# Kernel tuning notes

Measured on AMD Instinct MI355X. Metric: run time of the kernel, lower is better.

The kernel has to match this reference:

```python
import jax, jax.numpy as jnp
import numpy as np

E = 128       # embed_size
H = 256       # hidden_size
Q = 256       # query_size
B = 256       # batch size
N_ENT = 200000
N_REL = 500
N_NODES = 100000   # existing (head) nodes
N_NEW = 50000      # new tail nodes (segment_sum size)
M = 200000         # edges


def setup_inputs() -> dict:
    key = jax.random.key(0)
    ks = jax.random.split(key, 32)
    s = 0.02
    inp = {
        'entity_emb':   jax.random.normal(ks[0], (N_ENT, E), jnp.float32),
        'relation_emb': jax.random.normal(ks[1], (N_REL, E), jnp.float32),
        'node_hidden':  jax.random.normal(ks[2], (N_NODES, H), jnp.float32),
        'query_repr':   jax.random.normal(ks[3], (B, Q), jnp.float32),
        # attention params (Ws_attn, Wr_attn, Wqr_attn, w_alpha)
        'Ws':  jax.random.normal(ks[4], (H, H), jnp.float32) * s,
        'Wr':  jax.random.normal(ks[5], (E, H), jnp.float32) * s,
        'Wqr': jax.random.normal(ks[6], (E, H), jnp.float32) * s,
        'bqr': jnp.zeros((H,), jnp.float32),
        'w_alpha': jax.random.normal(ks[7], (H, 1), jnp.float32) * s,
        'b_alpha': jnp.zeros((1,), jnp.float32),
        # GRUCell (input = 2E message, hidden = H), torch layout [3H, in]
        'W_ih': jax.random.normal(ks[8], (3 * H, 2 * E), jnp.float32) * s,
        'W_hh': jax.random.normal(ks[9], (3 * H, H), jnp.float32) * s,
        'b_ih': jnp.zeros((3 * H,), jnp.float32),
        'b_hh': jnp.zeros((3 * H,), jnp.float32),
        # We2h: entity embed -> initial hidden
        'We2h_W': jax.random.normal(ks[10], (E, H), jnp.float32) * s,
        'We2h_b': jnp.zeros((H,), jnp.float32),
        # candidate_layer: [2E + H] -> H (agent_num = 1)
        'cand_W': jax.random.normal(ks[11], (2 * E + H, H), jnp.float32) * s,
        'cand_b': jnp.zeros((H,), jnp.float32),
        # rank_layer: [H + Q] -> 1
        'rank_W': jax.random.normal(ks[12], (H + Q, 1), jnp.float32) * s,
        'rank_b': jnp.zeros((1,), jnp.float32),
        # LayerNorm
        'ln_g': jnp.ones((H,), jnp.float32),
        'ln_b': jnp.zeros((H,), jnp.float32),
        # edge list (int constants)
        'head_node':     jax.random.randint(ks[13], (M,), 0, N_NODES, jnp.int32),
        'edge_rel':      jax.random.randint(ks[14], (M,), 0, N_REL, jnp.int32),
        'tail_ent':      jax.random.randint(ks[15], (M,), 0, N_ENT, jnp.int32),
        'tail_node':     jax.random.randint(ks[16], (M,), 0, N_NEW, jnp.int32),
        'query_rel':     jax.random.randint(ks[17], (M,), 0, N_REL, jnp.int32),
        'batch_idx':     jax.random.randint(ks[18], (M,), 0, B, jnp.int32),
        'tail_node_ent': jax.random.randint(ks[19], (N_NEW,), 0, N_ENT, jnp.int32),
    }
    return inp


def reference(entity_emb, relation_emb, node_hidden, query_repr,
              Ws, Wr, Wqr, bqr, w_alpha, b_alpha,
              W_ih, W_hh, b_ih, b_hh, We2h_W, We2h_b,
              cand_W, cand_b, rank_W, rank_b, ln_g, ln_b,
              head_node, edge_rel, tail_ent, tail_node, query_rel,
              batch_idx, tail_node_ent):
    lrelu = lambda x: jax.nn.leaky_relu(x, 0.01)
    # --- per-edge attention: w_alpha(ReLU(Ws h_s + Wr h_r + Wqr h_q)) ---
    hs = node_hidden[head_node]            # [M, H]
    hr = relation_emb[edge_rel]            # [M, E]
    hq = relation_emb[query_rel]           # [M, E]
    attn_feat = jax.nn.relu(hs @ Ws + hr @ Wr + hq @ Wqr + bqr)   # [M, H]
    alpha = jax.nn.sigmoid(attn_feat @ w_alpha + b_alpha)         # [M, 1]
    # --- attention-weighted message (rel || tail entity) scattered to tails ---
    te = entity_emb[tail_ent]                                     # [M, E]
    msg = jnp.concatenate([hr, te], axis=-1) * alpha              # [M, 2E]
    agg = jax.ops.segment_sum(msg, tail_node, num_segments=N_NEW) # [N_NEW, 2E]
    # --- GRUCell update of tail-node hidden states ---
    h_prev = lrelu(entity_emb[tail_node_ent] @ We2h_W + We2h_b)   # [N_NEW, H]
    gx = agg @ W_ih.T + b_ih                                      # [N_NEW, 3H]
    gh = h_prev @ W_hh.T + b_hh
    xr, xz, xn = jnp.split(gx, 3, axis=-1)
    hr_, hz_, hn_ = jnp.split(gh, 3, axis=-1)
    r = jax.nn.sigmoid(xr + hr_)
    z = jax.nn.sigmoid(xz + hz_)
    n = jnp.tanh(xn + r * hn_)
    h_new = (1.0 - z) * n + z * h_prev                            # [N_NEW, H]
    mu = jnp.mean(h_new, axis=-1, keepdims=True)
    var = jnp.var(h_new, axis=-1, keepdims=True)
    h_new = (h_new - mu) * jax.lax.rsqrt(var + 1e-5) * ln_g + ln_b
    # --- candidate scoring: candidate_layer + rank_layer ---
    cand_in = jnp.concatenate([te, hr, h_new[tail_node]], axis=-1)   # [M, 2E+H]
    cand_h = lrelu(cand_in @ cand_W + cand_b)                        # [M, H]
    rank_in = jnp.concatenate([cand_h, query_repr[batch_idx]], -1)   # [M, H+Q]
    scores = (rank_in @ rank_W + rank_b)[:, 0]                       # [M]
    return scores
```

## Files before the change

### kernel.cpp

```cpp
#include <hip/hip_runtime.h>
#include <math.h>


#define ACT_NONE 0
#define ACT_LRELU 1

typedef __attribute__((ext_vector_type(8))) short short8;
typedef __attribute__((ext_vector_type(4))) float floatx4;

__device__ __forceinline__ ushort f2b(float x) {
    union { float f; unsigned u; } v; v.f = x;
    return (ushort)((v.u + 0x7fffu + ((v.u >> 16) & 1u)) >> 16);
}
__device__ __forceinline__ float b2f(ushort b) {
    union { unsigned u; float f; } v; v.u = ((unsigned)b) << 16;
    return v.f;
}
__device__ __forceinline__ void gload16(const ushort* g, ushort* l) {
    __builtin_amdgcn_global_load_lds(
        (const __attribute__((address_space(1))) void*)g,
        (__attribute__((address_space(3))) void*)l, 16, 0, 0);
}

__global__ __launch_bounds__(256) void relprep_k(
    const float* __restrict__ A, const float* __restrict__ B0,
    const float* __restrict__ B1, const float* __restrict__ B2,
    float* __restrict__ C0, float* __restrict__ C1, ushort* __restrict__ C2,
    int M, int N, int K)
{
    __shared__ float As[16][68];
    __shared__ float Bs[16][68];
    const int z = blockIdx.z;
    const float* B = (z == 0) ? B0 : (z == 1) ? B1 : B2;
    const int tid = threadIdx.x;
    const int tx = tid & 15, ty = tid >> 4;
    const int m0 = blockIdx.x * 64, n0 = blockIdx.y * 64;
    float acc[4][4] = {};
    const int ar  = tid >> 2;
    const int ac4 = (tid & 3) * 4;
    const int brow = tid >> 4;
    const int bc4  = (tid & 15) * 4;
    const int gm = m0 + ar;
    const float* Arow = (gm < M) ? (A + (size_t)gm * K) : nullptr;
    for (int k0 = 0; k0 < K; k0 += 16) {
        float4 av = make_float4(0.f, 0.f, 0.f, 0.f);
        if (Arow) av = *(const float4*)(Arow + k0 + ac4);
        As[ac4 + 0][ar] = av.x;
        As[ac4 + 1][ar] = av.y;
        As[ac4 + 2][ar] = av.z;
        As[ac4 + 3][ar] = av.w;
        float4 bv = *(const float4*)(B + (size_t)(k0 + brow) * N + n0 + bc4);
        *(float4*)&Bs[brow][bc4] = bv;
        __syncthreads();
        #pragma unroll
        for (int kk = 0; kk < 16; ++kk) {
            float4 a4 = *(float4*)&As[kk][ty << 2];
            float4 b4 = *(float4*)&Bs[kk][tx << 2];
            float avr[4] = {a4.x, a4.y, a4.z, a4.w};
            float bvr[4] = {b4.x, b4.y, b4.z, b4.w};
            #pragma unroll
            for (int i = 0; i < 4; ++i)
                #pragma unroll
                for (int j = 0; j < 4; ++j)
                    acc[i][j] = fmaf(avr[i], bvr[j], acc[i][j]);
        }
        __syncthreads();
    }
    const int n = n0 + (tx << 2);
    #pragma unroll
    for (int i = 0; i < 4; ++i) {
        int m = m0 + (ty << 2) + i;
        if (m >= M) continue;
        if (z == 2) {
            ushort4 u;
            u.x = f2b(acc[i][0]); u.y = f2b(acc[i][1]);
            u.z = f2b(acc[i][2]); u.w = f2b(acc[i][3]);
            *(ushort4*)(C2 + (size_t)m * N + n) = u;
        } else {
            float* C = (z == 0) ? C0 : C1;
            *(float4*)(C + (size_t)m * N + n) =
                make_float4(acc[i][0], acc[i][1], acc[i][2], acc[i][3]);
        }
    }
}

__global__ __launch_bounds__(256) void convert16_k(
    const float* __restrict__ in, ushort* __restrict__ out, int n)
{
    int i = blockIdx.x * 256 + threadIdx.x;
    if (i < n) out[i] = f2b(in[i]);
}
__global__ __launch_bounds__(256) void transpose16_k(
    const float* __restrict__ in, ushort* __restrict__ out, int k0, int KS, int N)
{
    int i = blockIdx.x * 256 + threadIdx.x;
    if (i >= KS * N) return;
    int k = i / N, n = i - k * N;
    out[(size_t)n * KS + k] = f2b(in[(size_t)(k0 + k) * N + n]);
}

__global__ __launch_bounds__(256) void gemm16p_k(
    const ushort* __restrict__ A16, const int* __restrict__ a_idx,
    const ushort* __restrict__ BT, const float* __restrict__ bias,
    float* __restrict__ C, ushort* __restrict__ C16,
    int M, int N, int K, int act)
{
    __shared__ ushort As[2][128 * 32];
    __shared__ ushort Bs[2][128 * 32];
    const int tid = threadIdx.x;
    const int l = tid & 63, w = tid >> 6;
    const int m0 = blockIdx.y * 128, n0 = blockIdx.x * 128;

    const ushort* agp[2];
    const ushort* bgp[2];
    #pragma unroll
    for (int j = 0; j < 2; ++j) {
        int row = j * 64 + w * 16 + (l >> 2);
        int seg = (l & 3) ^ (row & 3);
        int r = m0 + row; if (r >= M) r = M - 1;
        int rr = a_idx ? a_idx[r] : r;
        agp[j] = A16 + (size_t)rr * K + seg * 8;
        bgp[j] = BT + (size_t)(n0 + row) * K + seg * 8;
    }

    const int wm = (w & 1) * 64, wn = (w >> 1) * 64;
    const int cl = l & 15, q = l >> 4;
    const int sseg = (q ^ (cl & 3)) * 8;
    const int aoff = (wm + cl) * 32 + sseg;
    const int boff = (wn + cl) * 32 + sseg;

    floatx4 acc[4][4];
    #pragma unroll
    for (int mi = 0; mi < 4; ++mi)
        #pragma unroll
        for (int ni = 0; ni < 4; ++ni) acc[mi][ni] = 0.f;

    const int NT = K >> 5;
    #pragma unroll
    for (int j = 0; j < 2; ++j) {
        gload16(agp[j], &As[0][j * 2048 + w * 512]);
        gload16(bgp[j], &Bs[0][j * 2048 + w * 512]);
    }
    __syncthreads();

    int buf = 0;
    for (int t = 0; t < NT; ++t) {
        if (t + 1 < NT) {
            int k0 = (t + 1) * 32;
            #pragma unroll
            for (int j = 0; j < 2; ++j) {
                gload16(agp[j] + k0, &As[buf ^ 1][j * 2048 + w * 512]);
                gload16(bgp[j] + k0, &Bs[buf ^ 1][j * 2048 + w * 512]);
            }
        }
        short8 af[4], bf[4];
        #pragma unroll
        for (int mi = 0; mi < 4; ++mi) af[mi] = *(short8*)&As[buf][aoff + mi * 512];
        #pragma unroll
        for (int ni = 0; ni < 4; ++ni) bf[ni] = *(short8*)&Bs[buf][boff + ni * 512];
        #pragma unroll
        for (int mi = 0; mi < 4; ++mi)
            #pragma unroll
            for (int ni = 0; ni < 4; ++ni)
                acc[mi][ni] = __builtin_amdgcn_mfma_f32_16x16x32_bf16(
                    bf[ni], af[mi], acc[mi][ni], 0, 0, 0);
        __syncthreads();
        buf ^= 1;
    }

    #pragma unroll
    for (int mi = 0; mi < 4; ++mi) {
        int row = m0 + wm + mi * 16 + cl;
        if (row >= M) continue;
        #pragma unroll
        for (int ni = 0; ni < 4; ++ni) {
            int col = n0 + wn + ni * 16 + q * 4;
            float4 bv = bias ? *(const float4*)(bias + col)
                             : make_float4(0.f, 0.f, 0.f, 0.f);
            float v[4];
            #pragma unroll
            for (int r = 0; r < 4; ++r) {
                float x = acc[mi][ni][r] + ((const float*)&bv)[r];
                if (act == ACT_LRELU) x = x > 0.f ? x : 0.01f * x;
                v[r] = x;
            }
            if (C16) {
                ushort4 u;
                u.x = f2b(v[0]); u.y = f2b(v[1]); u.z = f2b(v[2]); u.w = f2b(v[3]);
                *(ushort4*)(C16 + (size_t)row * N + col) = u;
            }
            if (C) *(float4*)(C + (size_t)row * N + col) =
                       make_float4(v[0], v[1], v[2], v[3]);
        }
    }
}

__global__ __launch_bounds__(256) void gemm16pw_k(
    const float* __restrict__ A, const ushort* __restrict__ BT,
    const float* __restrict__ bias, ushort* __restrict__ C16,
    int M, int K, int act)
{
    __shared__ ushort As[2][64 * 36];
    __shared__ ushort Bs[2][256 * 32];
    const int tid = threadIdx.x;
    const int l = tid & 63, w = tid >> 6;
    const int m0 = blockIdx.x * 64;

    const int ar = tid >> 2, af4 = tid & 3;
    int rr = m0 + ar; if (rr >= M) rr = M - 1;
    const float* agp = A + (size_t)rr * K + af4 * 8;
    const int awadr = ar * 36 + af4 * 8;

    const ushort* bgp[4];
    #pragma unroll
    for (int j = 0; j < 4; ++j) {
        int row = j * 64 + w * 16 + (l >> 2);
        int seg = (l & 3) ^ (row & 3);
        bgp[j] = BT + (size_t)row * K + seg * 8;
    }

    const int cl = l & 15, q = l >> 4;
    const int aoff = cl * 36 + q * 8;
    const int boff = (w * 64 + cl) * 32 + (q ^ (cl & 3)) * 8;

    floatx4 acc[4][4];
    #pragma unroll
    for (int mi = 0; mi < 4; ++mi)
        #pragma unroll
        for (int ni = 0; ni < 4; ++ni) acc[mi][ni] = 0.f;

    const int NT = K >> 5;
    #pragma unroll
    for (int j = 0; j < 4; ++j)
        gload16(bgp[j], &Bs[0][j * 2048 + w * 512]);
    {
        float4 v0 = *(const float4*)(agp);
        float4 v1 = *(const float4*)(agp + 4);
        ushort4 u0, u1;
        u0.x = f2b(v0.x); u0.y = f2b(v0.y); u0.z = f2b(v0.z); u0.w = f2b(v0.w);
        u1.x = f2b(v1.x); u1.y = f2b(v1.y); u1.z = f2b(v1.z); u1.w = f2b(v1.w);
        *(ushort4*)&As[0][awadr] = u0;
        *(ushort4*)&As[0][awadr + 4] = u1;
    }
    __syncthreads();

    int buf = 0;
    for (int t = 0; t < NT; ++t) {
        float4 v0, v1;
        if (t + 1 < NT) {
            int k0 = (t + 1) * 32;
            #pragma unroll
            for (int j = 0; j < 4; ++j)
                gload16(bgp[j] + k0, &Bs[buf ^ 1][j * 2048 + w * 512]);
            v0 = *(const float4*)(agp + k0);
            v1 = *(const float4*)(agp + k0 + 4);
        }
        short8 bf[4];
        #pragma unroll
        for (int ni = 0; ni < 4; ++ni) bf[ni] = *(short8*)&Bs[buf][boff + ni * 512];
        #pragma unroll
        for (int mi = 0; mi < 4; ++mi) {
            short8 af = *(short8*)&As[buf][aoff + mi * 576];
            #pragma unroll
            for (int ni = 0; ni < 4; ++ni)
                acc[mi][ni] = __builtin_amdgcn_mfma_f32_16x16x32_bf16(
                    bf[ni], af, acc[mi][ni], 0, 0, 0);
        }
        if (t + 1 < NT) {
            ushort4 u0, u1;
            u0.x = f2b(v0.x); u0.y = f2b(v0.y); u0.z = f2b(v0.z); u0.w = f2b(v0.w);
            u1.x = f2b(v1.x); u1.y = f2b(v1.y); u1.z = f2b(v1.z); u1.w = f2b(v1.w);
            *(ushort4*)&As[buf ^ 1][awadr] = u0;
            *(ushort4*)&As[buf ^ 1][awadr + 4] = u1;
        }
        __syncthreads();
        buf ^= 1;
    }

    #pragma unroll
    for (int mi = 0; mi < 4; ++mi) {
        int row = m0 + mi * 16 + cl;
        if (row >= M) continue;
        #pragma unroll
        for (int ni = 0; ni < 4; ++ni) {
            int col = w * 64 + ni * 16 + q * 4;
            float4 bv = bias ? *(const float4*)(bias + col)
                             : make_float4(0.f, 0.f, 0.f, 0.f);
            ushort4 u;
            float x0 = acc[mi][ni][0] + bv.x;
            float x1 = acc[mi][ni][1] + bv.y;
            float x2 = acc[mi][ni][2] + bv.z;
            float x3 = acc[mi][ni][3] + bv.w;
            if (act == ACT_LRELU) {
                x0 = x0 > 0.f ? x0 : 0.01f * x0;
                x1 = x1 > 0.f ? x1 : 0.01f * x1;
                x2 = x2 > 0.f ? x2 : 0.01f * x2;
                x3 = x3 > 0.f ? x3 : 0.01f * x3;
            }
            u.x = f2b(x0); u.y = f2b(x1); u.z = f2b(x2); u.w = f2b(x3);
            *(ushort4*)(C16 + (size_t)row * 256 + col) = u;
        }
    }
}

__global__ __launch_bounds__(256) void qdot_k(
    const float* __restrict__ q, const float* __restrict__ rank_W,
    float* __restrict__ qdot)
{
    int b = blockIdx.x * 4 + (threadIdx.x >> 6);
    int l = threadIdx.x & 63;
    float s = 0.f;
    #pragma unroll
    for (int k = 0; k < 4; ++k) {
        int h = l + k * 64;
        s += q[(size_t)b * 256 + h] * rank_W[256 + h];
    }
    #pragma unroll
    for (int off = 32; off; off >>= 1) s += __shfl_xor(s, off, 64);
    if (l == 0) qdot[b] = s;
}

__global__ __launch_bounds__(256) void alpha_k(
    const ushort* __restrict__ nodeWs16, const float* __restrict__ relWr,
    const float* __restrict__ relWqr, const float* __restrict__ bqr,
    const float* __restrict__ w_alpha, const float* __restrict__ b_alpha_p,
    const int* __restrict__ hcsr_hn, const int* __restrict__ hcsr_er,
    const int* __restrict__ hcsr_qr, const int* __restrict__ hcsr_e,
    float* __restrict__ alpha_out)
{
    const int tid = threadIdx.x;
    const int e0 = blockIdx.x * 32;
    __shared__ int hn[32], er[32], qr[32], se[32];
    if (tid < 32) {
        int i = e0 + tid;
        hn[tid] = hcsr_hn[i]; er[tid] = hcsr_er[i];
        qr[tid] = hcsr_qr[i]; se[tid] = hcsr_e[i];
    }
    __syncthreads();
    const int tx = tid & 63, ty = tid >> 6;
    const int c = tx * 4;
    const float4 bq = *(const float4*)(bqr + c);
    const float4 wa = *(const float4*)(w_alpha + c);
    float part[8];
    #pragma unroll
    for (int i2 = 0; i2 < 8; ++i2) {
        int i = ty * 8 + i2;
        ushort4 a16 = *(const ushort4*)(nodeWs16 + (size_t)hn[i] * 256 + c);
        float4 b = *(const float4*)(relWr + (size_t)er[i] * 256 + c);
        float4 d = *(const float4*)(relWqr + (size_t)qr[i] * 256 + c);
        float x0 = fmaxf(b2f(a16.x) + b.x + d.x + bq.x, 0.f);
        float x1 = fmaxf(b2f(a16.y) + b.y + d.y + bq.y, 0.f);
        float x2 = fmaxf(b2f(a16.z) + b.z + d.z + bq.z, 0.f);
        float x3 = fmaxf(b2f(a16.w) + b.w + d.w + bq.w, 0.f);
        part[i2] = x0 * wa.x + x1 * wa.y + x2 * wa.z + x3 * wa.w;
    }
    #pragma unroll
    for (int off = 32; off; off >>= 1)
        #pragma unroll
        for (int i2 = 0; i2 < 8; ++i2)
            part[i2] += __shfl_xor(part[i2], off, 64);
    if (tx == 0) {
        float ba = b_alpha_p[0];
        #pragma unroll
        for (int i2 = 0; i2 < 8; ++i2)
            alpha_out[se[ty * 8 + i2]] = 1.f / (1.f + __expf(-(part[i2] + ba)));
    }
}

__global__ __launch_bounds__(256) void hist2_k(
    const int* __restrict__ tail_node, const int* __restrict__ head_node,
    int* __restrict__ deg_t, int* __restrict__ deg_h, int M)
{
    int e = blockIdx.x * 256 + threadIdx.x;
    if (e < M) {
        atomicAdd(&deg_t[tail_node[e]], 1);
        atomicAdd(&deg_h[head_node[e]], 1);
    }
}
__global__ __launch_bounds__(512) void scan1_k(
    const int* __restrict__ deg, int* __restrict__ partial, int N)
{
    __shared__ int sm[512];
    int i = blockIdx.x * 512 + threadIdx.x;
    sm[threadIdx.x] = (i < N) ? deg[i] : 0;
    __syncthreads();
    for (int off = 256; off; off >>= 1) {
        if (threadIdx.x < off) sm[threadIdx.x] += sm[threadIdx.x + off];
        __syncthreads();
    }
    if (threadIdx.x == 0) partial[blockIdx.x] = sm[0];
}
__global__ __launch_bounds__(256) void scan2_k(
    int* __restrict__ partial, int nPart, int* __restrict__ offsets, int N, int M)
{
    __shared__ int sm[256];
    int t = threadIdx.x;
    int v = (t < nPart) ? partial[t] : 0;
    sm[t] = v;
    __syncthreads();
    for (int off = 1; off < 256; off <<= 1) {
        int add = (t >= off) ? sm[t - off] : 0;
        __syncthreads();
        sm[t] += add;
        __syncthreads();
    }
    if (t < nPart) partial[t] = sm[t] - v;
    if (t == 0) offsets[N] = M;
}
__global__ __launch_bounds__(512) void scan3_k(
    const int* __restrict__ deg, const int* __restrict__ partial,
    int* __restrict__ offsets, int* __restrict__ cursor, int N)
{
    __shared__ int sm[512];
    int i = blockIdx.x * 512 + threadIdx.x;
    int t = threadIdx.x;
    int v = (i < N) ? deg[i] : 0;
    sm[t] = v;
    __syncthreads();
    for (int off = 1; off < 512; off <<= 1) {
        int add = (t >= off) ? sm[t - off] : 0;
        __syncthreads();
        sm[t] += add;
        __syncthreads();
    }
    if (i < N) {
        int excl = partial[blockIdx.x] + sm[t] - v;
        offsets[i] = excl;
        cursor[i] = excl;
    }
}
__global__ __launch_bounds__(256) void fill_k(
    const int* __restrict__ tail_node, const int* __restrict__ tail_ent,
    const int* __restrict__ edge_rel, const int* __restrict__ batch_idx,
    int* __restrict__ cursor, int* __restrict__ ce, int* __restrict__ cte,
    int* __restrict__ cer, int* __restrict__ ctn, int* __restrict__ cbi, int M)
{
    int e = blockIdx.x * 256 + threadIdx.x;
    if (e < M) {
        int tn = tail_node[e];
        int pos = atomicAdd(&cursor[tn], 1);
        ce[pos] = e; cte[pos] = tail_ent[e]; cer[pos] = edge_rel[e];
        ctn[pos] = tn; cbi[pos] = batch_idx[e];
    }
}
__global__ __launch_bounds__(256) void hfill_k(
    const int* __restrict__ head_node, const int* __restrict__ edge_rel,
    const int* __restrict__ query_rel, int* __restrict__ cursor,
    int* __restrict__ hhn, int* __restrict__ her, int* __restrict__ hqr,
    int* __restrict__ he, int M)
{
    int e = blockIdx.x * 256 + threadIdx.x;
    if (e < M) {
        int h = head_node[e];
        int pos = atomicAdd(&cursor[h], 1);
        hhn[pos] = h; her[pos] = edge_rel[e]; hqr[pos] = query_rel[e]; he[pos] = e;
    }
}

__global__ __launch_bounds__(256) void agg_csr_k(
    const float* __restrict__ relation_emb, const ushort* __restrict__ ent16,
    const float* __restrict__ alpha, const int* __restrict__ csr_e,
    const int* __restrict__ csr_er, const int* __restrict__ csr_te,
    const int* __restrict__ offsets, ushort* __restrict__ agg16)
{
    int node = blockIdx.x * 4 + (threadIdx.x >> 6);
    int lane = threadIdx.x & 63;
    int beg = offsets[node], end = offsets[node + 1];
    float4 acc = make_float4(0.f, 0.f, 0.f, 0.f);
    const int c = lane * 4;
    for (int j = beg; j < end; ++j) {
        float a = alpha[csr_e[j]];
        float4 v;
        if (lane < 32) {
            v = *(const float4*)(relation_emb + (size_t)csr_er[j] * 128 + c);
        } else {
            ushort4 u = *(const ushort4*)(ent16 + (size_t)csr_te[j] * 128 + (c - 128));
            v = make_float4(b2f(u.x), b2f(u.y), b2f(u.z), b2f(u.w));
        }
        acc.x += v.x * a; acc.y += v.y * a;
        acc.z += v.z * a; acc.w += v.w * a;
    }
    ushort4 o;
    o.x = f2b(acc.x); o.y = f2b(acc.y); o.z = f2b(acc.z); o.w = f2b(acc.w);
    *(ushort4*)(agg16 + (size_t)node * 256 + c) = o;
}

__global__ __launch_bounds__(256) void gru_ln_k(
    const ushort* __restrict__ gx, const ushort* __restrict__ gh,
    const ushort* __restrict__ h_prev, const float* __restrict__ ln_g,
    const float* __restrict__ ln_b, ushort* __restrict__ h_new16, int n0)
{
    int nl = blockIdx.x * 4 + (threadIdx.x >> 6);
    int lane = threadIdx.x & 63;
    int n = n0 + nl;
    const ushort* gxr = gx + (size_t)nl * 768;
    const ushort* ghr = gh + (size_t)nl * 768;
    const ushort* hpr = h_prev + (size_t)n * 256;
    float hv[4]; float s = 0.f, s2 = 0.f;
    #pragma unroll
    for (int q2 = 0; q2 < 4; ++q2) {
        int h = lane + q2 * 64;
        float xr = b2f(gxr[h]), xz = b2f(gxr[256 + h]), xn = b2f(gxr[512 + h]);
        float hr_ = b2f(ghr[h]), hn_ = b2f(ghr[512 + h]);
        float hz_ = b2f(ghr[256 + h]);
        float hp = b2f(hpr[h]);
        float r = 1.f / (1.f + __expf(-(xr + hr_)));
        float z = 1.f / (1.f + __expf(-(xz + hz_)));
        float nn = tanhf(xn + r * hn_);
        float v = (1.f - z) * nn + z * hp;
        hv[q2] = v; s += v; s2 += v * v;
    }
    #pragma unroll
    for (int off = 32; off; off >>= 1) {
        s  += __shfl_xor(s, off, 64);
        s2 += __shfl_xor(s2, off, 64);
    }
    float mean = s * (1.f / 256.f);
    float var  = s2 * (1.f / 256.f) - mean * mean;
    float rstd = rsqrtf(var + 1e-5f);
    ushort* outr = h_new16 + (size_t)n * 256;
    #pragma unroll
    for (int q2 = 0; q2 < 4; ++q2) {
        int h = lane + q2 * 64;
        outr[h] = f2b((hv[q2] - mean) * rstd * ln_g[h] + ln_b[h]);
    }
}

__global__ __launch_bounds__(256) void score_mfma_k(
    const ushort* __restrict__ ent16, const ushort* __restrict__ candW1T,
    const ushort* __restrict__ relCand16, const ushort* __restrict__ hnewCand16,
    const float* __restrict__ rank_W, const float* __restrict__ rank_b_p,
    const float* __restrict__ qdot,
    const int* __restrict__ csr_e, const int* __restrict__ csr_te,
    const int* __restrict__ csr_er, const int* __restrict__ csr_tn,
    const int* __restrict__ csr_bi, float* __restrict__ scores)
{
    __shared__ ushort As[64 * 136];
    __shared__ int s_er[64], s_tn[64];
    __shared__ float s_part[4][64];
    const int tid = threadIdx.x;
    const int e0 = blockIdx.x * 64;
    __shared__ int s_te[64];
    if (tid < 64) {
        int idx = e0 + tid;
        s_te[tid] = csr_te[idx];
        s_er[tid] = csr_er[idx];
        s_tn[tid] = csr_tn[idx];
    }
    __syncthreads();

    {
        const int row = tid >> 2, s0 = tid & 3;
        const ushort* ar = ent16 + (size_t)s_te[row] * 128;
        #pragma unroll
        for (int j = 0; j < 4; ++j) {
            int seg = s0 + j * 4;
            *(uint4*)&As[row * 136 + seg * 8] = *(const uint4*)(ar + seg * 8);
        }
    }
    __syncthreads();

    const int l = tid & 63, w = tid >> 6;
    const int cl = l & 15, q = l >> 4;

    floatx4 acc[4][4];
    #pragma unroll
    for (int mi = 0; mi < 4; ++mi)
        #pragma unroll
        for (int ni = 0; ni < 4; ++ni) acc[mi][ni] = 0.f;

    const ushort* bbase = candW1T + (size_t)(w * 64 + cl) * 128 + q * 8;

    for (int k0 = 0; k0 < 128; k0 += 32) {
        short8 af[4], bf[4];
        #pragma unroll
        for (int ni = 0; ni < 4; ++ni)
            bf[ni] = *(const short8*)(bbase + ni * 2048 + k0);
        #pragma unroll
        for (int mi = 0; mi < 4; ++mi)
            af[mi] = *(short8*)&As[(mi * 16 + cl) * 136 + k0 + q * 8];
        #pragma unroll
        for (int mi = 0; mi < 4; ++mi)
            #pragma unroll
            for (int ni = 0; ni < 4; ++ni)
                acc[mi][ni] = __builtin_amdgcn_mfma_f32_16x16x32_bf16(
                    bf[ni], af[mi], acc[mi][ni], 0, 0, 0);
    }

    float rowsum[4];
    #pragma unroll
    for (int mi = 0; mi < 4; ++mi) {
        int row = mi * 16 + cl;
        int er = s_er[row], tn = s_tn[row];
        float rs = 0.f;
        #pragma unroll
        for (int ni = 0; ni < 4; ++ni) {
            int col = w * 64 + ni * 16 + q * 4;
            ushort4 rc = *(const ushort4*)(relCand16 + (size_t)er * 256 + col);
            ushort4 hc = *(const ushort4*)(hnewCand16 + (size_t)tn * 256 + col);
            float4 rw = *(const float4*)(rank_W + col);
            float v0 = acc[mi][ni][0] + b2f(rc.x) + b2f(hc.x);
            float v1 = acc[mi][ni][1] + b2f(rc.y) + b2f(hc.y);
            float v2 = acc[mi][ni][2] + b2f(rc.z) + b2f(hc.z);
            float v3 = acc[mi][ni][3] + b2f(rc.w) + b2f(hc.w);
            v0 = v0 > 0.f ? v0 : 0.01f * v0;
            v1 = v1 > 0.f ? v1 : 0.01f * v1;
            v2 = v2 > 0.f ? v2 : 0.01f * v2;
            v3 = v3 > 0.f ? v3 : 0.01f * v3;
            rs += v0 * rw.x + v1 * rw.y + v2 * rw.z + v3 * rw.w;
        }
        rowsum[mi] = rs;
    }
    #pragma unroll
    for (int mi = 0; mi < 4; ++mi) {
        rowsum[mi] += __shfl_xor(rowsum[mi], 16, 64);
        rowsum[mi] += __shfl_xor(rowsum[mi], 32, 64);
    }
    if (q == 0) {
        #pragma unroll
        for (int mi = 0; mi < 4; ++mi)
            s_part[w][mi * 16 + cl] = rowsum[mi];
    }
    __syncthreads();
    if (tid < 64) {
        int idx = e0 + tid;
        float s = s_part[0][tid] + s_part[1][tid] + s_part[2][tid] + s_part[3][tid]
                + qdot[csr_bi[idx]] + rank_b_p[0];
        scores[csr_e[idx]] = s;
    }
}

extern "C" void kernel_launch(void* const* d_in, const int* in_sizes, int n_in,
                              void* d_out, int out_size, void* d_ws, size_t ws_size,
                              hipStream_t stream)
{
    const float* entity_emb   = (const float*)d_in[0];
    const float* relation_emb = (const float*)d_in[1];
    const float* node_hidden  = (const float*)d_in[2];
    const float* query_repr   = (const float*)d_in[3];
    const float* Ws    = (const float*)d_in[4];
    const float* Wr    = (const float*)d_in[5];
    const float* Wqr   = (const float*)d_in[6];
    const float* bqr   = (const float*)d_in[7];
    const float* w_alpha = (const float*)d_in[8];
    const float* b_alpha = (const float*)d_in[9];
    const float* W_ih  = (const float*)d_in[10];
    const float* W_hh  = (const float*)d_in[11];
    const float* b_ih  = (const float*)d_in[12];
    const float* b_hh  = (const float*)d_in[13];
    const float* We2h_W = (const float*)d_in[14];
    const float* We2h_b = (const float*)d_in[15];
    const float* cand_W = (const float*)d_in[16];
    const float* cand_b = (const float*)d_in[17];
    const float* rank_W = (const float*)d_in[18];
    const float* rank_b = (const float*)d_in[19];
    const float* ln_g  = (const float*)d_in[20];
    const float* ln_b  = (const float*)d_in[21];
    const int* head_node = (const int*)d_in[22];
    const int* edge_rel  = (const int*)d_in[23];
    const int* tail_ent  = (const int*)d_in[24];
    const int* tail_node = (const int*)d_in[25];
    const int* query_rel = (const int*)d_in[26];
    const int* batch_idx = (const int*)d_in[27];
    const int* tail_node_ent = (const int*)d_in[28];
    float* out = (float*)d_out;
    (void)in_sizes; (void)n_in; (void)out_size; (void)ws_size;

    const int M = 200000, NNEW = 50000, NNODES = 100000, NREL = 500;
    const int NENT = 200000, E = 128;
    const int NCHUNK = 2, NC = NNEW / NCHUNK;
    const int NP_T = (NNEW + 511) / 512;
    const int NP_H = (NNODES + 511) / 512;

    float* w = (float*)d_ws;
    float* relWr    = w; w += NREL * 256;
    float* relWqr   = w; w += NREL * 256;
    float* qdot     = w; w += 256;
    float* alpha    = w; w += M;
    ushort* h_prev16   = (ushort*)w; w += (size_t)NNEW * 256 / 2;
    ushort* agg16      = (ushort*)w; w += (size_t)NNEW * 256 / 2;
    ushort* hnewCand16 = (ushort*)w; w += (size_t)NNEW * 256 / 2;
    ushort* relCand16  = (ushort*)w; w += (NREL * 256) / 2;
    ushort* ent16      = (ushort*)w; w += (size_t)NENT * E / 2;
    ushort* h_new16    = (ushort*)w; w += (size_t)NNEW * 256 / 2;
    ushort* W_ih16    = (ushort*)w; w += (768 * 256) / 2;
    ushort* W_hh16    = (ushort*)w; w += (768 * 256) / 2;
    ushort* WsT16     = (ushort*)w; w += (256 * 256) / 2;
    ushort* We2hT16   = (ushort*)w; w += (256 * 128) / 2;
    ushort* candW1T16 = (ushort*)w; w += (256 * 128) / 2;
    ushort* candW3T16 = (ushort*)w; w += (256 * 256) / 2;
    int* deg      = (int*)w; w += NNEW;
    int* offsets  = (int*)w; w += NNEW + 1;
    int* cursor   = (int*)w; w += NNEW;
    int* deg2     = (int*)w; w += NNODES;
    int* offsets2 = (int*)w; w += NNODES + 1;
    int* cursor2  = (int*)w; w += NNODES;
    int* partial  = (int*)w; w += 512;
    int* csr_e  = (int*)w; w += M;
    int* csr_te = (int*)w; w += M;
    int* csr_er = (int*)w; w += M;
    int* csr_tn = (int*)w; w += M;
    int* csr_bi = (int*)w; w += M;
    int* hcsr_hn = (int*)w; w += M;
    int* hcsr_er = (int*)w; w += M;
    int* hcsr_qr = (int*)w; w += M;
    int* hcsr_e  = (int*)w; w += M;
    w = (float*)(((uintptr_t)w + 63) & ~(uintptr_t)63);
    float* big = w;
    ushort* nodeWs16 = (ushort*)big;
    ushort* gx16 = (ushort*)big;
    ushort* gh16 = (ushort*)big + (size_t)NC * 768;

    hipMemsetAsync(deg, 0, NNEW * sizeof(int), stream);
    hipMemsetAsync(deg2, 0, NNODES * sizeof(int), stream);
    hist2_k<<<(M + 255) / 256, 256, 0, stream>>>(tail_node, head_node, deg, deg2, M);
    scan1_k<<<NP_T, 512, 0, stream>>>(deg, partial, NNEW);
    scan2_k<<<1, 256, 0, stream>>>(partial, NP_T, offsets, NNEW, M);
    scan3_k<<<NP_T, 512, 0, stream>>>(deg, partial, offsets, cursor, NNEW);
    fill_k<<<(M + 255) / 256, 256, 0, stream>>>(tail_node, tail_ent, edge_rel,
        batch_idx, cursor, csr_e, csr_te, csr_er, csr_tn, csr_bi, M);
    scan1_k<<<NP_H, 512, 0, stream>>>(deg2, partial, NNODES);
    scan2_k<<<1, 256, 0, stream>>>(partial, NP_H, offsets2, NNODES, M);
    scan3_k<<<NP_H, 512, 0, stream>>>(deg2, partial, offsets2, cursor2, NNODES);
    hfill_k<<<(M + 255) / 256, 256, 0, stream>>>(head_node, edge_rel, query_rel,
        cursor2, hcsr_hn, hcsr_er, hcsr_qr, hcsr_e, M);

    convert16_k<<<(NENT * E + 255) / 256, 256, 0, stream>>>(entity_emb, ent16, NENT * E);
    convert16_k<<<768, 256, 0, stream>>>(W_ih, W_ih16, 768 * 256);
    convert16_k<<<768, 256, 0, stream>>>(W_hh, W_hh16, 768 * 256);
    transpose16_k<<<256, 256, 0, stream>>>(Ws, WsT16, 0, 256, 256);
    transpose16_k<<<128, 256, 0, stream>>>(We2h_W, We2hT16, 0, 128, 256);
    transpose16_k<<<128, 256, 0, stream>>>(cand_W, candW1T16, 0, 128, 256);
    transpose16_k<<<256, 256, 0, stream>>>(cand_W, candW3T16, 256, 256, 256);
    relprep_k<<<dim3(8, 4, 3), 256, 0, stream>>>(
        relation_emb, Wr, Wqr, cand_W + 128 * 256,
        relWr, relWqr, relCand16, NREL, 256, 128);
    qdot_k<<<64, 256, 0, stream>>>(query_repr, rank_W, qdot);

    gemm16pw_k<<<(NNODES + 63) / 64, 256, 0, stream>>>(
        node_hidden, WsT16, nullptr, nodeWs16, NNODES, 256, ACT_NONE);

    alpha_k<<<M / 32, 256, 0, stream>>>(nodeWs16, relWr, relWqr, bqr, w_alpha, b_alpha,
                                        hcsr_hn, hcsr_er, hcsr_qr, hcsr_e, alpha);

    agg_csr_k<<<NNEW / 4, 256, 0, stream>>>(relation_emb, ent16, alpha,
                                            csr_e, csr_er, csr_te, offsets, agg16);

    gemm16p_k<<<dim3(2, (NNEW + 127) / 128), 256, 0, stream>>>(
        ent16, tail_node_ent, We2hT16, We2h_b, nullptr, h_prev16, NNEW, 256, 128, ACT_LRELU);

    for (int ch = 0; ch < NCHUNK; ++ch) {
        int n0 = ch * NC;
        gemm16p_k<<<dim3(6, (NC + 127) / 128), 256, 0, stream>>>(
            agg16 + (size_t)n0 * 256, nullptr, W_ih16, b_ih, nullptr, gx16, NC, 768, 256, ACT_NONE);
        gemm16p_k<<<dim3(6, (NC + 127) / 128), 256, 0, stream>>>(
            h_prev16 + (size_t)n0 * 256, nullptr, W_hh16, b_hh, nullptr, gh16, NC, 768, 256, ACT_NONE);
        gru_ln_k<<<NC / 4, 256, 0, stream>>>(gx16, gh16, h_prev16, ln_g, ln_b, h_new16, n0);
    }

    gemm16p_k<<<dim3(2, (NNEW + 127) / 128), 256, 0, stream>>>(
        h_new16, nullptr, candW3T16, cand_b, nullptr, hnewCand16, NNEW, 256, 256, ACT_NONE);

    score_mfma_k<<<M / 64, 256, 0, stream>>>(
        ent16, candW1T16, relCand16, hnewCand16, rank_W, rank_b, qdot,
        csr_e, csr_te, csr_er, csr_tn, csr_bi, out);
}
```

Before: 821.5 us.

## Fuse GRU/LayerNorm with candidate GEMM, batch weight prep, and prefetch in scoring

```diff
diff --git a/kernel.cpp b/kernel.cpp
--- a/kernel.cpp
+++ b/kernel.cpp
@@ -90,9 +90,28 @@
     int i = blockIdx.x * 256 + threadIdx.x;
     if (i < n) out[i] = f2b(in[i]);
 }
-__global__ __launch_bounds__(256) void transpose16_k(
-    const float* __restrict__ in, ushort* __restrict__ out, int k0, int KS, int N)
-{
+__global__ __launch_bounds__(256) void convertW_k(
+    const float* __restrict__ a, const float* __restrict__ b,
+    ushort* __restrict__ oa, ushort* __restrict__ ob)
+{
+    int i = blockIdx.x * 256 + threadIdx.x;
+    const int n = 768 * 256;
+    if (i < n) oa[i] = f2b(a[i]);
+    else       ob[i - n] = f2b(b[i - n]);
+}
+__global__ __launch_bounds__(256) void transpose4_k(
+    const float* __restrict__ Ws, const float* __restrict__ We2h,
+    const float* __restrict__ candW,
+    ushort* __restrict__ WsT, ushort* __restrict__ We2hT,
+    ushort* __restrict__ c1T, ushort* __restrict__ c3T)
+{
+    const int y = blockIdx.y;
+    const float* in; ushort* out; int k0, KS;
+    const int N = 256;
+    if (y == 0)      { in = Ws;    out = WsT;   k0 = 0;   KS = 256; }
+    else if (y == 1) { in = We2h;  out = We2hT; k0 = 0;   KS = 128; }
+    else if (y == 2) { in = candW; out = c1T;   k0 = 0;   KS = 128; }
+    else             { in = candW; out = c3T;   k0 = 256; KS = 256; }
     int i = blockIdx.x * 256 + threadIdx.x;
     if (i >= KS * N) return;
     int k = i / N, n = i - k * N;
@@ -468,7 +487,26 @@
     int beg = offsets[node], end = offsets[node + 1];
     float4 acc = make_float4(0.f, 0.f, 0.f, 0.f);
     const int c = lane * 4;
-    for (int j = beg; j < end; ++j) {
+    int j = beg;
+    for (; j + 1 < end; j += 2) {
+        float a0 = alpha[csr_e[j]];
+        float a1 = alpha[csr_e[j + 1]];
+        float4 v0, v1;
+        if (lane < 32) {
+            v0 = *(const float4*)(relation_emb + (size_t)csr_er[j] * 128 + c);
+            v1 = *(const float4*)(relation_emb + (size_t)csr_er[j + 1] * 128 + c);
+        } else {
+            ushort4 u0 = *(const ushort4*)(ent16 + (size_t)csr_te[j] * 128 + (c - 128));
+            ushort4 u1 = *(const ushort4*)(ent16 + (size_t)csr_te[j + 1] * 128 + (c - 128));
+            v0 = make_float4(b2f(u0.x), b2f(u0.y), b2f(u0.z), b2f(u0.w));
+            v1 = make_float4(b2f(u1.x), b2f(u1.y), b2f(u1.z), b2f(u1.w));
+        }
+        acc.x += v0.x * a0 + v1.x * a1;
+        acc.y += v0.y * a0 + v1.y * a1;
+        acc.z += v0.z * a0 + v1.z * a1;
+        acc.w += v0.w * a0 + v1.w * a1;
+    }
+    if (j < end) {
         float a = alpha[csr_e[j]];
         float4 v;
         if (lane < 32) {
@@ -485,44 +523,104 @@
     *(ushort4*)(agg16 + (size_t)node * 256 + c) = o;
 }
 
-__global__ __launch_bounds__(256) void gru_ln_k(
+__global__ __launch_bounds__(256) void gruln_cand_k(
     const ushort* __restrict__ gx, const ushort* __restrict__ gh,
     const ushort* __restrict__ h_prev, const float* __restrict__ ln_g,
-    const float* __restrict__ ln_b, ushort* __restrict__ h_new16, int n0)
-{
-    int nl = blockIdx.x * 4 + (threadIdx.x >> 6);
-    int lane = threadIdx.x & 63;
-    int n = n0 + nl;
-    const ushort* gxr = gx + (size_t)nl * 768;
-    const ushort* ghr = gh + (size_t)nl * 768;
-    const ushort* hpr = h_prev + (size_t)n * 256;
-    float hv[4]; float s = 0.f, s2 = 0.f;
-    #pragma unroll
-    for (int q2 = 0; q2 < 4; ++q2) {
-        int h = lane + q2 * 64;
-        float xr = b2f(gxr[h]), xz = b2f(gxr[256 + h]), xn = b2f(gxr[512 + h]);
-        float hr_ = b2f(ghr[h]), hn_ = b2f(ghr[512 + h]);
-        float hz_ = b2f(ghr[256 + h]);
-        float hp = b2f(hpr[h]);
-        float r = 1.f / (1.f + __expf(-(xr + hr_)));
-        float z = 1.f / (1.f + __expf(-(xz + hz_)));
-        float nn = tanhf(xn + r * hn_);
-        float v = (1.f - z) * nn + z * hp;
-        hv[q2] = v; s += v; s2 += v * v;
-    }
-    #pragma unroll
-    for (int off = 32; off; off >>= 1) {
-        s  += __shfl_xor(s, off, 64);
-        s2 += __shfl_xor(s2, off, 64);
-    }
-    float mean = s * (1.f / 256.f);
-    float var  = s2 * (1.f / 256.f) - mean * mean;
-    float rstd = rsqrtf(var + 1e-5f);
-    ushort* outr = h_new16 + (size_t)n * 256;
-    #pragma unroll
-    for (int q2 = 0; q2 < 4; ++q2) {
-        int h = lane + q2 * 64;
-        outr[h] = f2b((hv[q2] - mean) * rstd * ln_g[h] + ln_b[h]);
+    const float* __restrict__ ln_b, const float* __restrict__ cand_b,
+    const ushort* __restrict__ candW3T, ushort* __restrict__ hnewCand16,
+    int n0, int NC)
+{
+    __shared__ ushort Hs[64 * 264];
+    const int tid = threadIdx.x;
+    const int l = tid & 63, w = tid >> 6;
+    const int r0 = blockIdx.x * 64;
+
+    const float4 lg = *(const float4*)(ln_g + l * 4);
+    const float4 lb = *(const float4*)(ln_b + l * 4);
+    for (int p = 0; p < 16; ++p) {
+        int row = p * 4 + w;
+        int nl = r0 + row; if (nl >= NC) nl = NC - 1;
+        const ushort* gxr = gx + (size_t)nl * 768;
+        const ushort* ghr = gh + (size_t)nl * 768;
+        const ushort* hpr = h_prev + (size_t)(n0 + nl) * 256;
+        ushort4 xr4 = *(const ushort4*)(gxr + l * 4);
+        ushort4 xz4 = *(const ushort4*)(gxr + 256 + l * 4);
+        ushort4 xn4 = *(const ushort4*)(gxr + 512 + l * 4);
+        ushort4 hr4 = *(const ushort4*)(ghr + l * 4);
+        ushort4 hz4 = *(const ushort4*)(ghr + 256 + l * 4);
+        ushort4 hn4 = *(const ushort4*)(ghr + 512 + l * 4);
+        ushort4 hp4 = *(const ushort4*)(hpr + l * 4);
+        float hv[4]; float s = 0.f, s2 = 0.f;
+        #pragma unroll
+        for (int t = 0; t < 4; ++t) {
+            float xr = b2f(((const ushort*)&xr4)[t]);
+            float xz = b2f(((const ushort*)&xz4)[t]);
+            float xn = b2f(((const ushort*)&xn4)[t]);
+            float hr_ = b2f(((const ushort*)&hr4)[t]);
+            float hz_ = b2f(((const ushort*)&hz4)[t]);
+            float hn_ = b2f(((const ushort*)&hn4)[t]);
+            float hp = b2f(((const ushort*)&hp4)[t]);
+            float r = 1.f / (1.f + __expf(-(xr + hr_)));
+            float z = 1.f / (1.f + __expf(-(xz + hz_)));
+            float nn = tanhf(xn + r * hn_);
+            float v = (1.f - z) * nn + z * hp;
+            hv[t] = v; s += v; s2 += v * v;
+        }
+        #pragma unroll
+        for (int off = 32; off; off >>= 1) {
+            s  += __shfl_xor(s, off, 64);
+            s2 += __shfl_xor(s2, off, 64);
+        }
+        float mean = s * (1.f / 256.f);
+        float var  = s2 * (1.f / 256.f) - mean * mean;
+        float rstd = rsqrtf(var + 1e-5f);
+        ushort4 o;
+        o.x = f2b((hv[0] - mean) * rstd * lg.x + lb.x);
+        o.y = f2b((hv[1] - mean) * rstd * lg.y + lb.y);
+        o.z = f2b((hv[2] - mean) * rstd * lg.z + lb.z);
+        o.w = f2b((hv[3] - mean) * rstd * lg.w + lb.w);
+        *(ushort4*)&Hs[row * 264 + l * 4] = o;
+    }
+    __syncthreads();
+
+    const int cl = l & 15, q = l >> 4;
+    floatx4 acc[4][4];
+    #pragma unroll
+    for (int mi = 0; mi < 4; ++mi)
+        #pragma unroll
+        for (int ni = 0; ni < 4; ++ni) acc[mi][ni] = 0.f;
+
+    const ushort* bbase = candW3T + (size_t)(w * 64 + cl) * 256 + q * 8;
+    for (int k0 = 0; k0 < 256; k0 += 32) {
+        short8 af[4], bf[4];
+        #pragma unroll
+        for (int ni = 0; ni < 4; ++ni)
+            bf[ni] = *(const short8*)(bbase + ni * 4096 + k0);
+        #pragma unroll
+        for (int mi = 0; mi < 4; ++mi)
+            af[mi] = *(short8*)&Hs[(mi * 16 + cl) * 264 + k0 + q * 8];
+        #pragma unroll
+        for (int mi = 0; mi < 4; ++mi)
+            #pragma unroll
+            for (int ni = 0; ni < 4; ++ni)
+                acc[mi][ni] = __builtin_amdgcn_mfma_f32_16x16x32_bf16(
+                    bf[ni], af[mi], acc[mi][ni], 0, 0, 0);
+    }
+    #pragma unroll
+    for (int mi = 0; mi < 4; ++mi) {
+        int gr = r0 + mi * 16 + cl;
+        if (gr >= NC) continue;
+        #pragma unroll
+        for (int ni = 0; ni < 4; ++ni) {
+            int col = w * 64 + ni * 16 + q * 4;
+            float4 bv = *(const float4*)(cand_b + col);
+            ushort4 u;
+            u.x = f2b(acc[mi][ni][0] + bv.x);
+            u.y = f2b(acc[mi][ni][1] + bv.y);
+            u.z = f2b(acc[mi][ni][2] + bv.z);
+            u.w = f2b(acc[mi][ni][3] + bv.w);
+            *(ushort4*)(hnewCand16 + (size_t)(n0 + gr) * 256 + col) = u;
+        }
     }
 }
 
@@ -536,33 +634,37 @@
     const int* __restrict__ csr_bi, float* __restrict__ scores)
 {
     __shared__ ushort As[64 * 136];
-    __shared__ int s_er[64], s_tn[64];
     __shared__ float s_part[4][64];
     const int tid = threadIdx.x;
     const int e0 = blockIdx.x * 64;
-    __shared__ int s_te[64];
-    if (tid < 64) {
-        int idx = e0 + tid;
-        s_te[tid] = csr_te[idx];
-        s_er[tid] = csr_er[idx];
-        s_tn[tid] = csr_tn[idx];
-    }
-    __syncthreads();
+    const int l = tid & 63, w = tid >> 6;
+    const int cl = l & 15, q = l >> 4;
 
     {
         const int row = tid >> 2, s0 = tid & 3;
-        const ushort* ar = ent16 + (size_t)s_te[row] * 128;
+        const ushort* ar = ent16 + (size_t)csr_te[e0 + row] * 128;
         #pragma unroll
         for (int j = 0; j < 4; ++j) {
             int seg = s0 + j * 4;
             *(uint4*)&As[row * 136 + seg * 8] = *(const uint4*)(ar + seg * 8);
         }
     }
+    int er[4], tn[4];
+    #pragma unroll
+    for (int mi = 0; mi < 4; ++mi) {
+        int row = mi * 16 + cl;
+        er[mi] = csr_er[e0 + row];
+        tn[mi] = csr_tn[e0 + row];
+    }
+    ushort4 rc[2][4], hc[2][4];
+    #pragma unroll
+    for (int ni = 0; ni < 4; ++ni) {
+        int col = w * 64 + ni * 16 + q * 4;
+        rc[0][ni] = *(const ushort4*)(relCand16 + (size_t)er[0] * 256 + col);
+        hc[0][ni] = *(const ushort4*)(hnewCand16 + (size_t)tn[0] * 256 + col);
+    }
     __syncthreads();
 
-    const int l = tid & 63, w = tid >> 6;
-    const int cl = l & 15, q = l >> 4;
-
     floatx4 acc[4][4];
     #pragma unroll
     for (int mi = 0; mi < 4; ++mi)
@@ -570,7 +672,6 @@
         for (int ni = 0; ni < 4; ++ni) acc[mi][ni] = 0.f;
 
     const ushort* bbase = candW1T + (size_t)(w * 64 + cl) * 128 + q * 8;
-
     for (int k0 = 0; k0 < 128; k0 += 32) {
         short8 af[4], bf[4];
         #pragma unroll
@@ -587,27 +688,36 @@
                     bf[ni], af[mi], acc[mi][ni], 0, 0, 0);
     }
 
+    float4 rw[4];
+    #pragma unroll
+    for (int ni = 0; ni < 4; ++ni)
+        rw[ni] = *(const float4*)(rank_W + w * 64 + ni * 16 + q * 4);
+
     float rowsum[4];
     #pragma unroll
     for (int mi = 0; mi < 4; ++mi) {
-        int row = mi * 16 + cl;
-        int er = s_er[row], tn = s_tn[row];
+        if (mi < 3) {
+            int p = (mi + 1) & 1;
+            #pragma unroll
+            for (int ni = 0; ni < 4; ++ni) {
+                int col = w * 64 + ni * 16 + q * 4;
+                rc[p][ni] = *(const ushort4*)(relCand16 + (size_t)er[mi + 1] * 256 + col);
+                hc[p][ni] = *(const ushort4*)(hnewCand16 + (size_t)tn[mi + 1] * 256 + col);
+            }
+        }
+        const int p = mi & 1;
         float rs = 0.f;
         #pragma unroll
         for (int ni = 0; ni < 4; ++ni) {
-            int col = w * 64 + ni * 16 + q * 4;
-            ushort4 rc = *(const ushort4*)(relCand16 + (size_t)er * 256 + col);
-            ushort4 hc = *(const ushort4*)(hnewCand16 + (size_t)tn * 256 + col);
-            float4 rw = *(const float4*)(rank_W + col);
-            float v0 = acc[mi][ni][0] + b2f(rc.x) + b2f(hc.x);
-            float v1 = acc[mi][ni][1] + b2f(rc.y) + b2f(hc.y);
-            float v2 = acc[mi][ni][2] + b2f(rc.z) + b2f(hc.z);
-            float v3 = acc[mi][ni][3] + b2f(rc.w) + b2f(hc.w);
+            float v0 = acc[mi][ni][0] + b2f(rc[p][ni].x) + b2f(hc[p][ni].x);
+            float v1 = acc[mi][ni][1] + b2f(rc[p][ni].y) + b2f(hc[p][ni].y);
+            float v2 = acc[mi][ni][2] + b2f(rc[p][ni].z) + b2f(hc[p][ni].z);
+            float v3 = acc[mi][ni][3] + b2f(rc[p][ni].w) + b2f(hc[p][ni].w);
             v0 = v0 > 0.f ? v0 : 0.01f * v0;
             v1 = v1 > 0.f ? v1 : 0.01f * v1;
             v2 = v2 > 0.f ? v2 : 0.01f * v2;
             v3 = v3 > 0.f ? v3 : 0.01f * v3;
-            rs += v0 * rw.x + v1 * rw.y + v2 * rw.z + v3 * rw.w;
+            rs += v0 * rw[ni].x + v1 * rw[ni].y + v2 * rw[ni].z + v3 * rw[ni].w;
         }
         rowsum[mi] = rs;
     }
@@ -682,7 +792,6 @@
     ushort* hnewCand16 = (ushort*)w; w += (size_t)NNEW * 256 / 2;
     ushort* relCand16  = (ushort*)w; w += (NREL * 256) / 2;
     ushort* ent16      = (ushort*)w; w += (size_t)NENT * E / 2;
-    ushort* h_new16    = (ushort*)w; w += (size_t)NNEW * 256 / 2;
     ushort* W_ih16    = (ushort*)w; w += (768 * 256) / 2;
     ushort* W_hh16    = (ushort*)w; w += (768 * 256) / 2;
     ushort* WsT16     = (ushort*)w; w += (256 * 256) / 2;
@@ -726,12 +835,9 @@
         cursor2, hcsr_hn, hcsr_er, hcsr_qr, hcsr_e, M);
 
     convert16_k<<<(NENT * E + 255) / 256, 256, 0, stream>>>(entity_emb, ent16, NENT * E);
-    convert16_k<<<768, 256, 0, stream>>>(W_ih, W_ih16, 768 * 256);
-    convert16_k<<<768, 256, 0, stream>>>(W_hh, W_hh16, 768 * 256);
-    transpose16_k<<<256, 256, 0, stream>>>(Ws, WsT16, 0, 256, 256);
-    transpose16_k<<<128, 256, 0, stream>>>(We2h_W, We2hT16, 0, 128, 256);
-    transpose16_k<<<128, 256, 0, stream>>>(cand_W, candW1T16, 0, 128, 256);
-    transpose16_k<<<256, 256, 0, stream>>>(cand_W, candW3T16, 256, 256, 256);
+    convertW_k<<<1536, 256, 0, stream>>>(W_ih, W_hh, W_ih16, W_hh16);
+    transpose4_k<<<dim3(256, 4), 256, 0, stream>>>(
+        Ws, We2h_W, cand_W, WsT16, We2hT16, candW1T16, candW3T16);
     relprep_k<<<dim3(8, 4, 3), 256, 0, stream>>>(
         relation_emb, Wr, Wqr, cand_W + 128 * 256,
         relWr, relWqr, relCand16, NREL, 256, 128);
@@ -755,11 +861,9 @@
             agg16 + (size_t)n0 * 256, nullptr, W_ih16, b_ih, nullptr, gx16, NC, 768, 256, ACT_NONE);
         gemm16p_k<<<dim3(6, (NC + 127) / 128), 256, 0, stream>>>(
             h_prev16 + (size_t)n0 * 256, nullptr, W_hh16, b_hh, nullptr, gh16, NC, 768, 256, ACT_NONE);
-        gru_ln_k<<<NC / 4, 256, 0, stream>>>(gx16, gh16, h_prev16, ln_g, ln_b, h_new16, n0);
-    }
-
-    gemm16p_k<<<dim3(2, (NNEW + 127) / 128), 256, 0, stream>>>(
-        h_new16, nullptr, candW3T16, cand_b, nullptr, hnewCand16, NNEW, 256, 256, ACT_NONE);
+        gruln_cand_k<<<(NC + 63) / 64, 256, 0, stream>>>(
+            gx16, gh16, h_prev16, ln_g, ln_b, cand_b, candW3T16, hnewCand16, n0, NC);
+    }
 
     score_mfma_k<<<M / 64, 256, 0, stream>>>(
         ent16, candW1T16, relCand16, hnewCand16, rank_W, rank_b, qdot,
```

Measured after the change: 803.3 us. -2.2%, faster.
